# Kernel tuning notes

Hardware: AMD Instinct MI355X
Metric: run time of the kernel (lower is better)

Reference implementation:

```python
import jax, jax.numpy as jnp
import numpy as np
from jax import lax

N = 100000        # nodes
E = 3200000       # edges (avg degree 32)
F_IN = 128        # num_features
DIM = 16          # conv1 out
HID = 16          # conv2 out


def _gcn_layer(x, W, b, row, col, n):
    """PyG GCNConv: h = x @ W; add self-loops; symmetric deg^-1/2 norm;
    aggregate messages from source (row) at target (col); add bias."""
    h = x @ W                                   # [n, out]
    loop = jnp.arange(n)
    r = jnp.concatenate([row, loop])            # sources incl. self-loops
    c = jnp.concatenate([col, loop])            # targets incl. self-loops
    deg = jax.ops.segment_sum(jnp.ones(r.shape[0], dtype=h.dtype), c, num_segments=n)
    dinv = jnp.where(deg > 0, lax.rsqrt(deg), jnp.zeros((), h.dtype))
    norm = dinv[r] * dinv[c]                    # [E+n]
    out = jax.ops.segment_sum(h[r] * norm[:, None], c, num_segments=n)
    return out + b


def setup_inputs() -> dict:
    key = jax.random.key(0)
    k1, k2, k3, k4, k5, k6 = jax.random.split(key, 6)
    x = jax.random.normal(k1, (N, F_IN), dtype=jnp.float32)
    edge_index = jax.random.randint(k2, (2, E), 0, N, dtype=jnp.int64)
    # GCNConv weights (glorot-ish scale) and zero-init biases (PyG default init style)
    W1 = jax.random.normal(k3, (F_IN, DIM), dtype=jnp.float32) * (1.0 / np.sqrt(F_IN))
    b1 = jnp.zeros((DIM,), dtype=jnp.float32)
    W2 = jax.random.normal(k4, (DIM, HID), dtype=jnp.float32) * (1.0 / np.sqrt(DIM))
    b2 = jnp.zeros((HID,), dtype=jnp.float32)
    return {"x": x, "edge_index": edge_index, "W1": W1, "b1": b1, "W2": W2, "b2": b2}


def reference(x, edge_index, W1, b1, W2, b2):
    row, col = edge_index[0], edge_index[1]
    h = jax.nn.relu(_gcn_layer(x, W1, b1, row, col, N))
    out = jax.nn.relu(_gcn_layer(h, W2, b2, row, col, N))
    return out
```

## Files before the change

### kernel.cpp

```cpp
#include <hip/hip_runtime.h>
#include <hip/hip_fp16.h>

#define N_NODES 100000
#define N_EDGES 3200000
#define F_IN    128
#define DIM     16

#define SUP_SH  9
#define NSUP    196
#define SCAP    17920
#define CHA     4096
#define NBLKA   ((N_EDGES + CHA - 1) / CHA)
#define NCAP    96
#define GROWS   32
#define NBLKG   (N_NODES / GROWS)

static inline size_t alignup(size_t x) { return (x + 255) & ~(size_t)255; }

__global__ void zero_init(int* __restrict__ cursorA) {
    cursorA[threadIdx.x] = 0;
}

__global__ __launch_bounds__(512) void partA_gemm(const int* __restrict__ row,
                                                  const int* __restrict__ col,
                                                  int* __restrict__ cursorA,
                                                  unsigned* __restrict__ stageA,
                                                  const float* __restrict__ x,
                                                  const float* __restrict__ W,
                                                  __half* __restrict__ hu) {
    __shared__ __align__(16) char smem[25600];
    const int t = threadIdx.x;
    const int bid = blockIdx.x;

    if (bid % 5 == 0) {
        int* hist   = (int*)smem;
        int* lstart = hist + 256;
        int* lcur   = hist + 512;
        int* gbase  = hist + 768;
        int* scanT  = hist + 1024;
        unsigned* stg = (unsigned*)(smem + 5120);
        unsigned char* stgb = (unsigned char*)(smem + 21504);

        const int e0 = (bid / 5) * CHA;
        const int nv = min(CHA, N_EDGES - e0);
        const int i0 = t * 8;
        const bool act = (i0 < nv);

        if (t < 256) hist[t] = 0;

        int4 c0, c1, r0, r1;
        if (act) {
            c0 = *(const int4*)(col + e0 + i0);
            c1 = *(const int4*)(col + e0 + i0 + 4);
            r0 = *(const int4*)(row + e0 + i0);
            r1 = *(const int4*)(row + e0 + i0 + 4);
        }
        __syncthreads();
        if (act) {
            atomicAdd(&hist[(unsigned)c0.x >> SUP_SH], 1);
            atomicAdd(&hist[(unsigned)c0.y >> SUP_SH], 1);
            atomicAdd(&hist[(unsigned)c0.z >> SUP_SH], 1);
            atomicAdd(&hist[(unsigned)c0.w >> SUP_SH], 1);
            atomicAdd(&hist[(unsigned)c1.x >> SUP_SH], 1);
            atomicAdd(&hist[(unsigned)c1.y >> SUP_SH], 1);
            atomicAdd(&hist[(unsigned)c1.z >> SUP_SH], 1);
            atomicAdd(&hist[(unsigned)c1.w >> SUP_SH], 1);
        }
        __syncthreads();
        int v = 0;
        if (t < 256) { v = hist[t]; scanT[t] = v; }
        __syncthreads();
#pragma unroll
        for (int off = 1; off < 256; off <<= 1) {
            int a = (t >= off && t < 256) ? scanT[t - off] : 0;
            __syncthreads();
            if (t < 256) scanT[t] += a;
            __syncthreads();
        }
        if (t < 256) {
            int ex = scanT[t] - v;
            lstart[t] = ex; lcur[t] = ex;
            if (v) {
                int gb = atomicAdd(&cursorA[t], v);
                if (gb + v > SCAP) gb = SCAP - v;
                gbase[t] = t * SCAP + gb;
            }
        }
        __syncthreads();
        if (act) {
            int cc[8] = { c0.x, c0.y, c0.z, c0.w, c1.x, c1.y, c1.z, c1.w };
            int rr[8] = { r0.x, r0.y, r0.z, r0.w, r1.x, r1.y, r1.z, r1.w };
#pragma unroll
            for (int q = 0; q < 8; ++q) {
                int sp = (unsigned)cc[q] >> SUP_SH;
                int p = atomicAdd(&lcur[sp], 1);
                stg[p] = (unsigned)rr[q] | ((unsigned)(cc[q] & 511) << 17);
                stgb[p] = (unsigned char)sp;
            }
        }
        __syncthreads();
        for (int i = t; i < nv; i += 512) {
            int sp = stgb[i];
            stageA[gbase[sp] + (i - lstart[sp])] = stg[i];
        }
    } else {
        float4* sW4 = (float4*)smem;
        float4 (*sX4)[F_IN / 4 + 1] = (float4 (*)[F_IN / 4 + 1])(smem + 8192);
        const int gb = bid - bid / 5 - 1;
        const int base = gb * GROWS;
        sW4[t] = ((const float4*)W)[t];
#pragma unroll
        for (int i = t; i < GROWS * (F_IN / 4); i += 512) {
            int r = i >> 5, k4 = i & 31;
            sX4[r][k4] = ((const float4*)(x + (size_t)(base + r) * F_IN))[k4];
        }
        __syncthreads();
        const float* sW = (const float*)sW4;
        const int rrow = t >> 4, cj = t & 15;
        const float* xr = (const float*)&sX4[rrow][0];
        float acc = 0.f;
#pragma unroll
        for (int k = 0; k < F_IN; ++k) acc += xr[k] * sW[k * DIM + cj];
        hu[(size_t)(base + rrow) * DIM + cj] = __float2half(acc);
    }
}

__global__ __launch_bounds__(1024) void partB(const unsigned* __restrict__ stageA,
                                              const int* __restrict__ cursorA,
                                              int* __restrict__ nodeCur,
                                              unsigned* __restrict__ csr,
                                              const __half2* __restrict__ hu,
                                              __half2* __restrict__ hd) {
    __shared__ int lcur[512];
    __shared__ float dl[512];
    const int t = threadIdx.x;
    const int sup = blockIdx.x;
    const int nbase = sup << SUP_SH;
    if (t < 512) lcur[t] = (nbase + t) * NCAP;
    __syncthreads();
    const int base = sup * SCAP;
    const int cnt = min(cursorA[sup], SCAP);
    for (int i = t; i < cnt; i += 1024) {
        unsigned v = stageA[base + i];
        int n = (v >> 17) & 511;
        int pos = atomicAdd(&lcur[n], 1);
        if (pos < (nbase + n) * NCAP + NCAP)
            csr[pos] = (v & 0x1FFFFu) << 3;
    }
    __syncthreads();
    if (t < 512) {
        int node = nbase + t;
        if (node < N_NODES) {
            int deg = min(lcur[t] - node * NCAP, NCAP);
            nodeCur[node] = deg;
            dl[t] = rsqrtf((float)deg + 1.0f);
        }
    }
    __syncthreads();
    const int nn = min(N_NODES - nbase, 512);
    for (int idx = t; idx < nn * 8; idx += 1024) {
        int nl = idx >> 3, f = idx & 7;
        float2 vf = __half22float2(hu[(size_t)(nbase + nl) * 8 + f]);
        float d = dl[nl];
        hd[(size_t)(nbase + nl) * 8 + f] = __floats2half2_rn(vf.x * d, vf.y * d);
    }
}

__device__ __forceinline__ void node_gather(const unsigned* __restrict__ csr,
                                            const __half2* __restrict__ h2,
                                            int p, int end, int f,
                                            float& ax, float& ay) {
    for (; p + 15 < end; p += 16) {
        uint4 ea = *(const uint4*)(csr + p);
        uint4 eb = *(const uint4*)(csr + p + 4);
        uint4 ec = *(const uint4*)(csr + p + 8);
        uint4 ed = *(const uint4*)(csr + p + 12);
        __half2 g0 = h2[ea.x + f], g1 = h2[ea.y + f];
        __half2 g2 = h2[ea.z + f], g3 = h2[ea.w + f];
        __half2 g4 = h2[eb.x + f], g5 = h2[eb.y + f];
        __half2 g6 = h2[eb.z + f], g7 = h2[eb.w + f];
        __half2 g8 = h2[ec.x + f], g9 = h2[ec.y + f];
        __half2 ga = h2[ec.z + f], gb = h2[ec.w + f];
        __half2 gc = h2[ed.x + f], gd = h2[ed.y + f];
        __half2 ge = h2[ed.z + f], gf = h2[ed.w + f];
        float2 t0 = __half22float2(__hadd2(g0, g1));
        float2 t1 = __half22float2(__hadd2(g2, g3));
        float2 t2 = __half22float2(__hadd2(g4, g5));
        float2 t3 = __half22float2(__hadd2(g6, g7));
        float2 t4 = __half22float2(__hadd2(g8, g9));
        float2 t5 = __half22float2(__hadd2(ga, gb));
        float2 t6 = __half22float2(__hadd2(gc, gd));
        float2 t7 = __half22float2(__hadd2(ge, gf));
        ax += ((t0.x + t1.x) + (t2.x + t3.x)) + ((t4.x + t5.x) + (t6.x + t7.x));
        ay += ((t0.y + t1.y) + (t2.y + t3.y)) + ((t4.y + t5.y) + (t6.y + t7.y));
    }
    if (p + 7 < end) {
        uint4 ea = *(const uint4*)(csr + p);
        uint4 eb = *(const uint4*)(csr + p + 4);
        __half2 g0 = h2[ea.x + f], g1 = h2[ea.y + f];
        __half2 g2 = h2[ea.z + f], g3 = h2[ea.w + f];
        __half2 g4 = h2[eb.x + f], g5 = h2[eb.y + f];
        __half2 g6 = h2[eb.z + f], g7 = h2[eb.w + f];
        float2 t0 = __half22float2(__hadd2(g0, g1));
        float2 t1 = __half22float2(__hadd2(g2, g3));
        float2 t2 = __half22float2(__hadd2(g4, g5));
        float2 t3 = __half22float2(__hadd2(g6, g7));
        ax += (t0.x + t1.x) + (t2.x + t3.x);
        ay += (t0.y + t1.y) + (t2.y + t3.y);
        p += 8;
    }
    if (p + 3 < end) {
        uint4 e4 = *(const uint4*)(csr + p);
        __half2 g0 = h2[e4.x + f], g1 = h2[e4.y + f];
        __half2 g2 = h2[e4.z + f], g3 = h2[e4.w + f];
        float2 t0 = __half22float2(__hadd2(g0, g1));
        float2 t1 = __half22float2(__hadd2(g2, g3));
        ax += t0.x + t1.x;
        ay += t0.y + t1.y;
        p += 4;
    }
    for (; p < end; ++p) {
        float2 v = __half22float2(h2[csr[p] + f]);
        ax += v.x; ay += v.y;
    }
}

__global__ __launch_bounds__(256) void agg1(const unsigned* __restrict__ csr,
                                            const int* __restrict__ nodeCur,
                                            const __half2* __restrict__ hd,
                                            const float* __restrict__ b1,
                                            const float* __restrict__ W2,
                                            __half2* __restrict__ hd2) {
    __shared__ float sW2[DIM * DIM];
    __shared__ float sb1[DIM];
    const int t = threadIdx.x;
    sW2[t] = W2[t];
    if (t < DIM) sb1[t] = b1[t];
    __syncthreads();
    const int lane = t & 63, f = lane & 7;
    const int node = blockIdx.x * 32 + ((t >> 6) << 3) + (lane >> 3);
    const int degv = nodeCur[node];
    const float dc = rsqrtf((float)degv + 1.0f);
    const int p0 = node * NCAP;
    float ax = 0.f, ay = 0.f;
    node_gather(csr, hd, p0, p0 + degv, f, ax, ay);
    float2 sv = __half22float2(hd[(size_t)node * 8 + f]);
    float fx = dc * (ax + sv.x) + sb1[2 * f];
    float fy = dc * (ay + sv.y) + sb1[2 * f + 1];
    fx = fmaxf(fx, 0.f); fy = fmaxf(fy, 0.f);
    float sx = 0.f, sy = 0.f;
    const int gl = lane & 56;
#pragma unroll
    for (int mq = 0; mq < 8; ++mq) {
        float lo = __shfl(fx, gl + mq, 64);
        float hi = __shfl(fy, gl + mq, 64);
        sx += lo * sW2[(2 * mq) * DIM + 2 * f]     + hi * sW2[(2 * mq + 1) * DIM + 2 * f];
        sy += lo * sW2[(2 * mq) * DIM + 2 * f + 1] + hi * sW2[(2 * mq + 1) * DIM + 2 * f + 1];
    }
    hd2[(size_t)node * 8 + f] = __floats2half2_rn(dc * sx, dc * sy);
}

__global__ __launch_bounds__(256) void agg2(const unsigned* __restrict__ csr,
                                            const int* __restrict__ nodeCur,
                                            const __half2* __restrict__ hd2,
                                            const float* __restrict__ b2,
                                            float2* __restrict__ out2) {
    __shared__ float sb2[DIM];
    const int t = threadIdx.x;
    if (t < DIM) sb2[t] = b2[t];
    __syncthreads();
    const int lane = t & 63, f = lane & 7;
    const int node = blockIdx.x * 32 + ((t >> 6) << 3) + (lane >> 3);
    const int degv = nodeCur[node];
    const float dc = rsqrtf((float)degv + 1.0f);
    const int p0 = node * NCAP;
    float ax = 0.f, ay = 0.f;
    node_gather(csr, hd2, p0, p0 + degv, f, ax, ay);
    float2 sv = __half22float2(hd2[(size_t)node * 8 + f]);
    float fx = dc * (ax + sv.x) + sb2[2 * f];
    float fy = dc * (ay + sv.y) + sb2[2 * f + 1];
    out2[(size_t)node * 8 + f] = make_float2(fmaxf(fx, 0.f), fmaxf(fy, 0.f));
}

extern "C" void kernel_launch(void* const* d_in, const int* in_sizes, int n_in,
                              void* d_out, int out_size, void* d_ws, size_t ws_size,
                              hipStream_t stream) {
    const float* x   = (const float*)d_in[0];
    const int*   ei  = (const int*)d_in[1];
    const float* W1  = (const float*)d_in[2];
    const float* b1  = (const float*)d_in[3];
    const float* W2  = (const float*)d_in[4];
    const float* b2  = (const float*)d_in[5];
    float*       out = (float*)d_out;

    const int* row = ei;
    const int* col = ei + N_EDGES;

    char* ws = (char*)d_ws;
    size_t o = 0;
    auto take = [&](size_t bytes) { char* p = ws + o; o = alignup(o + bytes); return p; };
    int*      nodeCur = (int*)     take((size_t)N_NODES * 4);
    int*      cursorA = (int*)     take((size_t)256 * 4);
    unsigned* stageA  = (unsigned*)take((size_t)NSUP * SCAP * 4);
    unsigned* csr     = (unsigned*)take((size_t)N_NODES * NCAP * 4);
    __half*   hu      = (__half*)  take((size_t)N_NODES * DIM * 2);
    __half*   hd      = (__half*)  take((size_t)N_NODES * DIM * 2);
    __half*   hd2     = (__half*)  take((size_t)N_NODES * DIM * 2);

    zero_init<<<1, 256, 0, stream>>>(cursorA);
    partA_gemm<<<NBLKA + NBLKG, 512, 0, stream>>>(row, col, cursorA, stageA,
                                                  x, W1, hu);
    partB<<<NSUP, 1024, 0, stream>>>(stageA, cursorA, nodeCur, csr,
                                     (const __half2*)hu, (__half2*)hd);

    agg1<<<N_NODES / 32, 256, 0, stream>>>(csr, nodeCur, (const __half2*)hd,
                                           b1, W2, (__half2*)hd2);
    agg2<<<N_NODES / 32, 256, 0, stream>>>(csr, nodeCur, (const __half2*)hd2,
                                           b2, (float2*)out);
}
```

Baseline: 110.5 us.

## Fuse CSR build and both aggregations into one cooperative persistent kernel

Merges partB, agg1 and agg2 into a single cooperative kernel that uses grid-wide syncs between phases instead of separate launches, with a fallback to three separate 512-thread kernels. PartB now runs with 512 threads per block instead of 1024, and aggregation blocks cover 64 nodes instead of 32. The aim is to remove launch gaps and tail effects between the dependent stages. In exchange, partB gets only 196 blocks working while the rest of the grid waits at the barrier, grid.sync adds its own cost, and the grid is capped at 1024 blocks.

```diff
diff --git a/kernel.cpp b/kernel.cpp
--- a/kernel.cpp
+++ b/kernel.cpp
@@ -1,5 +1,8 @@
 #include <hip/hip_runtime.h>
 #include <hip/hip_fp16.h>
+#include <hip/hip_cooperative_groups.h>
+
+namespace cg = cooperative_groups;
 
 #define N_NODES 100000
 #define N_EDGES 3200000
@@ -14,6 +17,8 @@
 #define NCAP    96
 #define GROWS   32
 #define NBLKG   (N_NODES / GROWS)
+#define RATIO   5
+#define NGRP    ((N_NODES + 63) / 64)
 
 static inline size_t alignup(size_t x) { return (x + 255) & ~(size_t)255; }
 
@@ -32,7 +37,7 @@
     const int t = threadIdx.x;
     const int bid = blockIdx.x;
 
-    if (bid % 5 == 0) {
+    if (bid % RATIO == 0) {
         int* hist   = (int*)smem;
         int* lstart = hist + 256;
         int* lcur   = hist + 512;
@@ -41,7 +46,7 @@
         unsigned* stg = (unsigned*)(smem + 5120);
         unsigned char* stgb = (unsigned char*)(smem + 21504);
 
-        const int e0 = (bid / 5) * CHA;
+        const int e0 = (bid / RATIO) * CHA;
         const int nv = min(CHA, N_EDGES - e0);
         const int i0 = t * 8;
         const bool act = (i0 < nv);
@@ -106,7 +111,7 @@
     } else {
         float4* sW4 = (float4*)smem;
         float4 (*sX4)[F_IN / 4 + 1] = (float4 (*)[F_IN / 4 + 1])(smem + 8192);
-        const int gb = bid - bid / 5 - 1;
+        const int gb = bid - bid / RATIO - 1;
         const int base = gb * GROWS;
         sW4[t] = ((const float4*)W)[t];
 #pragma unroll
@@ -125,22 +130,21 @@
     }
 }
 
-__global__ __launch_bounds__(1024) void partB(const unsigned* __restrict__ stageA,
-                                              const int* __restrict__ cursorA,
-                                              int* __restrict__ nodeCur,
-                                              unsigned* __restrict__ csr,
-                                              const __half2* __restrict__ hu,
-                                              __half2* __restrict__ hd) {
-    __shared__ int lcur[512];
-    __shared__ float dl[512];
-    const int t = threadIdx.x;
-    const int sup = blockIdx.x;
+__device__ __forceinline__ void partB_body(const unsigned* __restrict__ stageA,
+                                           const int* __restrict__ cursorA,
+                                           int* __restrict__ nodeCur,
+                                           unsigned* __restrict__ csr,
+                                           const __half2* __restrict__ hu,
+                                           __half2* __restrict__ hd,
+                                           int sup, int t,
+                                           int* lcur, float* dl) {
+    __syncthreads();
     const int nbase = sup << SUP_SH;
-    if (t < 512) lcur[t] = (nbase + t) * NCAP;
+    lcur[t] = (nbase + t) * NCAP;
     __syncthreads();
     const int base = sup * SCAP;
     const int cnt = min(cursorA[sup], SCAP);
-    for (int i = t; i < cnt; i += 1024) {
+    for (int i = t; i < cnt; i += 512) {
         unsigned v = stageA[base + i];
         int n = (v >> 17) & 511;
         int pos = atomicAdd(&lcur[n], 1);
@@ -148,7 +152,7 @@
             csr[pos] = (v & 0x1FFFFu) << 3;
     }
     __syncthreads();
-    if (t < 512) {
+    {
         int node = nbase + t;
         if (node < N_NODES) {
             int deg = min(lcur[t] - node * NCAP, NCAP);
@@ -158,7 +162,7 @@
     }
     __syncthreads();
     const int nn = min(N_NODES - nbase, 512);
-    for (int idx = t; idx < nn * 8; idx += 1024) {
+    for (int idx = t; idx < nn * 8; idx += 512) {
         int nl = idx >> 3, f = idx & 7;
         float2 vf = __half22float2(hu[(size_t)(nbase + nl) * 8 + f]);
         float d = dl[nl];
@@ -225,20 +229,13 @@
     }
 }
 
-__global__ __launch_bounds__(256) void agg1(const unsigned* __restrict__ csr,
-                                            const int* __restrict__ nodeCur,
-                                            const __half2* __restrict__ hd,
-                                            const float* __restrict__ b1,
-                                            const float* __restrict__ W2,
-                                            __half2* __restrict__ hd2) {
-    __shared__ float sW2[DIM * DIM];
-    __shared__ float sb1[DIM];
-    const int t = threadIdx.x;
-    sW2[t] = W2[t];
-    if (t < DIM) sb1[t] = b1[t];
-    __syncthreads();
-    const int lane = t & 63, f = lane & 7;
-    const int node = blockIdx.x * 32 + ((t >> 6) << 3) + (lane >> 3);
+__device__ __forceinline__ void agg1_node(const unsigned* __restrict__ csr,
+                                          const int* __restrict__ nodeCur,
+                                          const __half2* __restrict__ hd,
+                                          const float* __restrict__ sW2,
+                                          const float* __restrict__ sb1,
+                                          __half2* __restrict__ hd2,
+                                          int node, int lane, int f) {
     const int degv = nodeCur[node];
     const float dc = rsqrtf((float)degv + 1.0f);
     const int p0 = node * NCAP;
@@ -260,17 +257,12 @@
     hd2[(size_t)node * 8 + f] = __floats2half2_rn(dc * sx, dc * sy);
 }
 
-__global__ __launch_bounds__(256) void agg2(const unsigned* __restrict__ csr,
-                                            const int* __restrict__ nodeCur,
-                                            const __half2* __restrict__ hd2,
-                                            const float* __restrict__ b2,
-                                            float2* __restrict__ out2) {
-    __shared__ float sb2[DIM];
-    const int t = threadIdx.x;
-    if (t < DIM) sb2[t] = b2[t];
-    __syncthreads();
-    const int lane = t & 63, f = lane & 7;
-    const int node = blockIdx.x * 32 + ((t >> 6) << 3) + (lane >> 3);
+__device__ __forceinline__ void agg2_node(const unsigned* __restrict__ csr,
+                                          const int* __restrict__ nodeCur,
+                                          const __half2* __restrict__ hd2,
+                                          const float* __restrict__ sb2,
+                                          float2* __restrict__ out2,
+                                          int node, int f) {
     const int degv = nodeCur[node];
     const float dc = rsqrtf((float)degv + 1.0f);
     const int p0 = node * NCAP;
@@ -280,6 +272,90 @@
     float fx = dc * (ax + sv.x) + sb2[2 * f];
     float fy = dc * (ay + sv.y) + sb2[2 * f + 1];
     out2[(size_t)node * 8 + f] = make_float2(fmaxf(fx, 0.f), fmaxf(fy, 0.f));
+}
+
+__global__ __launch_bounds__(512, 8) void net_fused(const unsigned* __restrict__ stageA,
+                                                    const int* __restrict__ cursorA,
+                                                    int* __restrict__ nodeCur,
+                                                    unsigned* __restrict__ csr,
+                                                    const __half2* __restrict__ hu,
+                                                    __half2* __restrict__ hd,
+                                                    __half2* __restrict__ hd2,
+                                                    const float* __restrict__ b1,
+                                                    const float* __restrict__ W2,
+                                                    const float* __restrict__ b2,
+                                                    float2* __restrict__ out2) {
+    __shared__ int   lcur[512];
+    __shared__ float dl[512];
+    __shared__ float sW2[DIM * DIM];
+    __shared__ float sb[DIM];
+    cg::grid_group grid = cg::this_grid();
+    const int t = threadIdx.x;
+    const int lane = t & 63, f = lane & 7;
+
+    for (int s = blockIdx.x; s < NSUP; s += gridDim.x)
+        partB_body(stageA, cursorA, nodeCur, csr, hu, hd, s, t, lcur, dl);
+    __threadfence();
+    grid.sync();
+
+    if (t < DIM * DIM) sW2[t] = W2[t];
+    if (t < DIM) sb[t] = b1[t];
+    __syncthreads();
+    for (int g = blockIdx.x; g < NGRP; g += gridDim.x) {
+        int node = g * 64 + ((t >> 6) << 3) + (lane >> 3);
+        if (node < N_NODES) agg1_node(csr, nodeCur, hd, sW2, sb, hd2, node, lane, f);
+    }
+    __threadfence();
+    grid.sync();
+
+    if (t < DIM) sb[t] = b2[t];
+    __syncthreads();
+    for (int g = blockIdx.x; g < NGRP; g += gridDim.x) {
+        int node = g * 64 + ((t >> 6) << 3) + (lane >> 3);
+        if (node < N_NODES) agg2_node(csr, nodeCur, hd2, sb, out2, node, f);
+    }
+}
+
+__global__ __launch_bounds__(512) void partB_k(const unsigned* __restrict__ stageA,
+                                               const int* __restrict__ cursorA,
+                                               int* __restrict__ nodeCur,
+                                               unsigned* __restrict__ csr,
+                                               const __half2* __restrict__ hu,
+                                               __half2* __restrict__ hd) {
+    __shared__ int lcur[512];
+    __shared__ float dl[512];
+    partB_body(stageA, cursorA, nodeCur, csr, hu, hd, blockIdx.x, threadIdx.x, lcur, dl);
+}
+
+__global__ __launch_bounds__(512) void agg1_k(const unsigned* __restrict__ csr,
+                                              const int* __restrict__ nodeCur,
+                                              const __half2* __restrict__ hd,
+                                              const float* __restrict__ b1,
+                                              const float* __restrict__ W2,
+                                              __half2* __restrict__ hd2) {
+    __shared__ float sW2[DIM * DIM];
+    __shared__ float sb[DIM];
+    const int t = threadIdx.x;
+    if (t < DIM * DIM) sW2[t] = W2[t];
+    if (t < DIM) sb[t] = b1[t];
+    __syncthreads();
+    const int lane = t & 63, f = lane & 7;
+    const int node = blockIdx.x * 64 + ((t >> 6) << 3) + (lane >> 3);
+    if (node < N_NODES) agg1_node(csr, nodeCur, hd, sW2, sb, hd2, node, lane, f);
+}
+
+__global__ __launch_bounds__(512) void agg2_k(const unsigned* __restrict__ csr,
+                                              const int* __restrict__ nodeCur,
+                                              const __half2* __restrict__ hd2,
+                                              const float* __restrict__ b2,
+                                              float2* __restrict__ out2) {
+    __shared__ float sb[DIM];
+    const int t = threadIdx.x;
+    if (t < DIM) sb[t] = b2[t];
+    __syncthreads();
+    const int lane = t & 63, f = lane & 7;
+    const int node = blockIdx.x * 64 + ((t >> 6) << 3) + (lane >> 3);
+    if (node < N_NODES) agg2_node(csr, nodeCur, hd2, sb, out2, node, f);
 }
 
 extern "C" void kernel_launch(void* const* d_in, const int* in_sizes, int n_in,
@@ -310,11 +386,33 @@
     zero_init<<<1, 256, 0, stream>>>(cursorA);
     partA_gemm<<<NBLKA + NBLKG, 512, 0, stream>>>(row, col, cursorA, stageA,
                                                   x, W1, hu);
-    partB<<<NSUP, 1024, 0, stream>>>(stageA, cursorA, nodeCur, csr,
-                                     (const __half2*)hu, (__half2*)hd);
-
-    agg1<<<N_NODES / 32, 256, 0, stream>>>(csr, nodeCur, (const __half2*)hd,
-                                           b1, W2, (__half2*)hd2);
-    agg2<<<N_NODES / 32, 256, 0, stream>>>(csr, nodeCur, (const __half2*)hd2,
-                                           b2, (float2*)out);
-}
+
+    const unsigned* stageA_c = stageA;
+    const int*      cursorA_c = cursorA;
+    const __half2*  hu_c  = (const __half2*)hu;
+    __half2*        hd_p  = (__half2*)hd;
+    __half2*        hd2_p = (__half2*)hd2;
+    float2*         out_p = (float2*)out;
+
+    bool coop_ok = false;
+    int maxB = 0;
+    if (hipOccupancyMaxActiveBlocksPerMultiprocessor(&maxB, (const void*)net_fused,
+                                                     512, 0) == hipSuccess && maxB > 0) {
+        int grid = maxB * 256;
+        if (grid > 1024) grid = 1024;
+        void* args[] = { (void*)&stageA_c, (void*)&cursorA_c, (void*)&nodeCur,
+                         (void*)&csr, (void*)&hu_c, (void*)&hd_p, (void*)&hd2_p,
+                         (void*)&b1, (void*)&W2, (void*)&b2, (void*)&out_p };
+        if (hipLaunchCooperativeKernel((const void*)net_fused, dim3(grid), dim3(512),
+                                       args, 0, stream) == hipSuccess)
+            coop_ok = true;
+    }
+    if (!coop_ok) {
+        partB_k<<<NSUP, 512, 0, stream>>>(stageA, cursorA, nodeCur, csr,
+                                          (const __half2*)hu, (__half2*)hd);
+        agg1_k<<<NGRP, 512, 0, stream>>>(csr, nodeCur, (const __half2*)hd,
+                                         b1, W2, (__half2*)hd2);
+        agg2_k<<<NGRP, 512, 0, stream>>>(csr, nodeCur, (const __half2*)hd2,
+                                         b2, (float2*)out);
+    }
+}
```

Measured after the change: 412.3 us. 273% more time.
